# Performance work log

Hardware: AMD Instinct MI355X
Metric: run time of the kernel (lower is better)

The kernel has to match this reference:

```python
import jax, jax.numpy as jnp
import numpy as np
import math

DIM = 4096
N_HEADS = 32
HEAD_DIM = DIM // N_HEADS  # 128


def setup_inputs() -> dict:
    key = jax.random.key(0)
    ks = jax.random.split(key, 10)
    B, S, C = 2, 1024, 2048
    x = jax.random.normal(ks[0], (B, S, DIM), dtype=jnp.float32)
    freqs_cis = jax.random.normal(ks[1], (S, HEAD_DIM // 2), dtype=jnp.float32)
    mask = jnp.zeros((1, 1, S, C), dtype=jnp.float32)
    input_idexes = jnp.arange(S, dtype=jnp.int64) if jax.config.jax_enable_x64 else jnp.arange(S, dtype=jnp.int32)
    cache_k = jax.random.normal(ks[2], (B, C, N_HEADS, HEAD_DIM), dtype=jnp.float32) * 0.1
    cache_v = jax.random.normal(ks[3], (B, C, N_HEADS, HEAD_DIM), dtype=jnp.float32) * 0.1
    # Linear weights in torch layout [out_features, in_features], y = x @ W.T
    wq = jax.random.normal(ks[4], (DIM, DIM), dtype=jnp.float32) * 0.02
    wk = jax.random.normal(ks[5], (DIM, DIM), dtype=jnp.float32) * 0.02
    wv = jax.random.normal(ks[6], (DIM, DIM), dtype=jnp.float32) * 0.02
    wo = jax.random.normal(ks[7], (DIM, DIM), dtype=jnp.float32) * 0.02
    return {"x": x, "freqs_cis": freqs_cis, "mask": mask, "input_idexes": input_idexes,
            "cache_k": cache_k, "cache_v": cache_v, "wq": wq, "wk": wk, "wv": wv, "wo": wo}


def reference(x, freqs_cis, mask, input_idexes, cache_k, cache_v, wq, wk, wv, wo):
    B, S, D = x.shape
    H, hd = N_HEADS, HEAD_DIM
    # projections (torch Linear: x @ W.T)
    xq = jnp.einsum('bsd,ed->bse', x, wq).reshape(B, S, H, hd)
    # xk/xv are computed in the original forward but never used (cache-only attention)
    xk = jnp.einsum('bsd,ed->bse', x, wk).reshape(B, S, H, hd)  # noqa: F841
    xv = jnp.einsum('bsd,ed->bse', x, wv).reshape(B, S, H, hd)  # noqa: F841
    q = xq.transpose(0, 2, 1, 3)                 # [B,H,S,hd]
    keys = cache_k.transpose(0, 2, 1, 3)         # [B,H,C,hd]
    values = cache_v.transpose(0, 2, 1, 3)       # [B,H,C,hd]
    scores = jnp.einsum('bhse,bhce->bhsc', q, keys) / math.sqrt(hd)
    scores = scores + mask
    attn = jax.nn.softmax(scores.astype(jnp.float32), axis=-1).astype(q.dtype)
    out = jnp.einsum('bhsc,bhce->bhse', attn, values)  # [B,H,S,hd]
    out = out.transpose(0, 2, 1, 3).reshape(B, S, H * hd)
    return jnp.einsum('bse,de->bsd', out, wo)
```

## Files before the change

### kernel.cpp

```cpp
#include <hip/hip_runtime.h>
#include <hip/hip_bf16.h>
#include <stdint.h>


#define DIM   4096
#define NH    32
#define HD    128
#define BB    2
#define SS    1024
#define CC    2048

typedef __bf16 bf16x8 __attribute__((ext_vector_type(8)));
typedef float  f32x4  __attribute__((ext_vector_type(4)));

__device__ __forceinline__ unsigned short f2bf(float f) {
  union { __hip_bfloat16 h; unsigned short u; } cv;
  cv.h = __float2bfloat16(f);
  return cv.u;
}

__device__ __forceinline__ void gl_lds16(const void* g, void* l) {
  __builtin_amdgcn_global_load_lds(
      (__attribute__((address_space(1))) void*)(uintptr_t)(g),
      (__attribute__((address_space(3))) void*)(l), 16, 0, 0);
}

__global__ void conv_f32_bf16(const float* __restrict__ in, unsigned short* __restrict__ out, int n4) {
  int i = blockIdx.x * blockDim.x + threadIdx.x;
  int stride = gridDim.x * blockDim.x;
  for (; i < n4; i += stride) {
    float4 v = reinterpret_cast<const float4*>(in)[i];
    ushort4 o;
    o.x = f2bf(v.x); o.y = f2bf(v.y); o.z = f2bf(v.z); o.w = f2bf(v.w);
    reinterpret_cast<ushort4*>(out)[i] = o;
  }
}

__global__ void conv_k(const float* __restrict__ in, unsigned short* __restrict__ out) {
  const int total4 = BB * NH * CC * HD / 4;
  int i = blockIdx.x * blockDim.x + threadIdx.x;
  int stride = gridDim.x * blockDim.x;
  for (; i < total4; i += stride) {
    size_t o = (size_t)i * 4;
    int d   = (int)(o & (HD - 1));
    size_t r = o >> 7;
    int c   = (int)(r & (CC - 1));
    int bh  = (int)(r >> 11);
    int hh = bh & (NH - 1), bb = bh >> 5;
    float4 v = *reinterpret_cast<const float4*>(in + ((size_t)(bb * CC + c) * NH + hh) * HD + d);
    ushort4 u; u.x = f2bf(v.x); u.y = f2bf(v.y); u.z = f2bf(v.z); u.w = f2bf(v.w);
    *reinterpret_cast<ushort4*>(out + o) = u;
  }
}

__global__ void conv_v_t(const float* __restrict__ in, unsigned short* __restrict__ out) {
  __shared__ float tile[32][33];
  const int c0 = blockIdx.x * 32, d0 = blockIdx.y * 32;
  const int bh = blockIdx.z;
  const int hh = bh & (NH - 1), bb = bh >> 5;
  const int tx = threadIdx.x, ty = threadIdx.y;
#pragma unroll
  for (int i = 0; i < 4; ++i) {
    int c = c0 + ty + i * 8;
    tile[ty + i * 8][tx] = in[((size_t)(bb * CC + c) * NH + hh) * HD + d0 + tx];
  }
  __syncthreads();
#pragma unroll
  for (int i = 0; i < 4; ++i) {
    int d = d0 + ty + i * 8;
    out[((size_t)bh * HD + d) * CC + c0 + tx] = f2bf(tile[tx][ty + i * 8]);
  }
}

template <int OUT_BF16>
__global__ __launch_bounds__(256, 2) void gemm_bt(
    const unsigned short* __restrict__ A,
    const unsigned short* __restrict__ Bw,
    void* __restrict__ Cout,
    int M, int N, int K, float scale)
{
  __shared__ __align__(16) unsigned short As[128 * 32];
  __shared__ __align__(16) unsigned short Bs[128 * 32];
  const int t = threadIdx.x;
  const int w = t >> 6, lane = t & 63;
  const int wr = w >> 1, wc = w & 1;
  const int bm0 = blockIdx.y * 128, bn0 = blockIdx.x * 128;

  const unsigned short* aSrc = A  + (size_t)(bm0 + (t >> 2)) * K + (t & 3) * 8;
  const unsigned short* bSrc = Bw + (size_t)(bn0 + (t >> 2)) * K + (t & 3) * 8;
  char* aDst = (char*)As + w * 1024;
  char* bDst = (char*)Bs + w * 1024;
  const size_t half = (size_t)64 * K;

  f32x4 acc[4][4];
#pragma unroll
  for (int m = 0; m < 4; ++m)
#pragma unroll
    for (int n = 0; n < 4; ++n) acc[m][n] = (f32x4){0.f, 0.f, 0.f, 0.f};

  for (int k0 = 0; k0 < K; k0 += 32) {
    gl_lds16(aSrc,        aDst);
    gl_lds16(aSrc + half, aDst + 4096);
    gl_lds16(bSrc,        bDst);
    gl_lds16(bSrc + half, bDst + 4096);
    aSrc += 32; bSrc += 32;
    __syncthreads();

    bf16x8 af[4], bf[4];
#pragma unroll
    for (int m = 0; m < 4; ++m)
      af[m] = *(const bf16x8*)&As[(wr * 64 + m * 16 + (lane & 15)) * 32 + (lane >> 4) * 8];
#pragma unroll
    for (int n = 0; n < 4; ++n)
      bf[n] = *(const bf16x8*)&Bs[(wc * 64 + n * 16 + (lane & 15)) * 32 + (lane >> 4) * 8];
#pragma unroll
    for (int m = 0; m < 4; ++m)
#pragma unroll
      for (int n = 0; n < 4; ++n)
        acc[m][n] = __builtin_amdgcn_mfma_f32_16x16x32_bf16(af[m], bf[n], acc[m][n], 0, 0, 0);
    __syncthreads();
  }

  const int r0 = (lane >> 4) * 4, cl = lane & 15;
#pragma unroll
  for (int m = 0; m < 4; ++m) {
#pragma unroll
    for (int n = 0; n < 4; ++n) {
      int row = bm0 + wr * 64 + m * 16 + r0;
      int col = bn0 + wc * 64 + n * 16 + cl;
#pragma unroll
      for (int r = 0; r < 4; ++r) {
        float v = acc[m][n][r] * scale;
        if (OUT_BF16) ((unsigned short*)Cout)[(size_t)(row + r) * N + col] = f2bf(v);
        else          ((float*)Cout)[(size_t)(row + r) * N + col] = v;
      }
    }
  }
}

__global__ __launch_bounds__(256, 2) void attn_fwd(
    const unsigned short* __restrict__ Qb,
    const unsigned short* __restrict__ Kb,
    const unsigned short* __restrict__ Vtb,
    const float* __restrict__ mask,
    unsigned short* __restrict__ Ob)
{
  __shared__ __align__(16) unsigned short Ks[2][64 * 128];
  __shared__ __align__(16) unsigned short Vs[2][64 * 128];
  __shared__ __align__(16) unsigned short Ps[4][16 * 64];

  const int t = threadIdx.x, w = t >> 6, lane = t & 63;
  const int bid = blockIdx.x;
  const int qt = bid & 15, bh = bid >> 4;
  const int hh = bh & (NH - 1), bb = bh >> 5;
  const int q0 = qt * 64;
  const int l15 = lane & 15, g = lane >> 4;
  const int rb4 = g * 4;

  bf16x8 qf[4];
  {
    const unsigned short* qp = Qb + ((size_t)(bb * SS + q0 + w * 16 + l15)) * DIM + hh * HD + g * 8;
#pragma unroll
    for (int kk = 0; kk < 4; ++kk)
      qf[kk] = *(const bf16x8*)(qp + kk * 32);
  }

  const unsigned short* kSrc = Kb + ((size_t)bh * CC + (t >> 4)) * HD
                               + (((t & 15) ^ ((t >> 4) & 7)) * 8);
  const unsigned short* vSrc = Vtb + ((size_t)bh * HD + (t >> 3)) * CC
                               + (((t & 7) ^ ((t >> 3) & 7)) * 8);

  f32x4 acc_o[8];
#pragma unroll
  for (int i = 0; i < 8; ++i) acc_o[i] = (f32x4){0.f, 0.f, 0.f, 0.f};
  float m_run[4], l_run[4];
#pragma unroll
  for (int r = 0; r < 4; ++r) { m_run[r] = -1e30f; l_run[r] = 0.f; }

  const int swz = (lane & 7) << 3;
  const float LOG2E = 1.4426950408889634f;

  {
    char* kd = (char*)Ks[0] + w * 1024;
    char* vd = (char*)Vs[0] + w * 1024;
#pragma unroll
    for (int i = 0; i < 4; ++i) {
      gl_lds16(kSrc + (size_t)(i * 16) * HD, kd + i * 4096);
      gl_lds16(vSrc + (size_t)i * 32 * CC,   vd + i * 4096);
    }
  }
  __syncthreads();

  int cur = 0;
  for (int c0 = 0; c0 < CC; c0 += 64) {
    if (c0 + 64 < CC) {
      char* kd = (char*)Ks[cur ^ 1] + w * 1024;
      char* vd = (char*)Vs[cur ^ 1] + w * 1024;
#pragma unroll
      for (int i = 0; i < 4; ++i) {
        gl_lds16(kSrc + (size_t)(c0 + 64 + i * 16) * HD, kd + i * 4096);
        gl_lds16(vSrc + (size_t)i * 32 * CC + c0 + 64,   vd + i * 4096);
      }
    }

    float mk[4][4];
#pragma unroll
    for (int nf = 0; nf < 4; ++nf)
#pragma unroll
      for (int r = 0; r < 4; ++r)
        mk[nf][r] = mask[(size_t)(q0 + w * 16 + rb4 + r) * CC + c0 + nf * 16 + l15];

    f32x4 sc[4];
#pragma unroll
    for (int nf = 0; nf < 4; ++nf) sc[nf] = (f32x4){0.f, 0.f, 0.f, 0.f};
    __builtin_amdgcn_s_setprio(1);
#pragma unroll
    for (int kk = 0; kk < 4; ++kk) {
#pragma unroll
      for (int nf = 0; nf < 4; ++nf) {
        bf16x8 kf = *(const bf16x8*)&Ks[cur][((nf * 16 + l15) * 128 + kk * 32 + g * 8) ^ swz];
        sc[nf] = __builtin_amdgcn_mfma_f32_16x16x32_bf16(qf[kk], kf, sc[nf], 0, 0, 0);
      }
    }
    __builtin_amdgcn_s_setprio(0);

#pragma unroll
    for (int nf = 0; nf < 4; ++nf)
#pragma unroll
      for (int r = 0; r < 4; ++r)
        sc[nf][r] = fmaf(mk[nf][r], LOG2E, sc[nf][r]);

    int ok = 1;
    float pm[4];
#pragma unroll
    for (int r = 0; r < 4; ++r) {
      pm[r] = fmaxf(fmaxf(sc[0][r], sc[1][r]), fmaxf(sc[2][r], sc[3][r]));
      ok = ok && (pm[r] <= m_run[r] + 8.0f);
    }
    if (!__all(ok)) {
#pragma unroll
      for (int r = 0; r < 4; ++r) {
        float mx = pm[r];
#pragma unroll
        for (int d = 1; d < 16; d <<= 1)
          mx = fmaxf(mx, __shfl_xor(mx, d));
        float mn = fmaxf(m_run[r], mx);
        float corr = __builtin_amdgcn_exp2f(m_run[r] - mn);
        m_run[r] = mn;
        l_run[r] *= corr;
#pragma unroll
        for (int nd = 0; nd < 8; ++nd) acc_o[nd][r] *= corr;
      }
    }

#pragma unroll
    for (int r = 0; r < 4; ++r) {
      int rw = rb4 + r;
      int rsw = (rw & 7) << 3;
#pragma unroll
      for (int nf = 0; nf < 4; ++nf) {
        float p = __builtin_amdgcn_exp2f(sc[nf][r] - m_run[r]);
        l_run[r] += p;
        Ps[w][rw * 64 + ((nf * 16 + l15) ^ rsw)] = f2bf(p);
      }
    }

    __builtin_amdgcn_s_setprio(1);
#pragma unroll
    for (int kk = 0; kk < 2; ++kk) {
      bf16x8 pf = *(const bf16x8*)&Ps[w][(l15 * 64 + kk * 32 + g * 8) ^ swz];
#pragma unroll
      for (int nd = 0; nd < 8; ++nd) {
        bf16x8 vf = *(const bf16x8*)&Vs[cur][((nd * 16 + l15) * 64 + kk * 32 + g * 8) ^ swz];
        acc_o[nd] = __builtin_amdgcn_mfma_f32_16x16x32_bf16(pf, vf, acc_o[nd], 0, 0, 0);
      }
    }
    __builtin_amdgcn_s_setprio(0);
    __syncthreads();
    cur ^= 1;
  }

#pragma unroll
  for (int r = 0; r < 4; ++r)
#pragma unroll
    for (int d = 1; d < 16; d <<= 1)
      l_run[r] += __shfl_xor(l_run[r], d);

#pragma unroll
  for (int nd = 0; nd < 8; ++nd)
#pragma unroll
    for (int r = 0; r < 4; ++r) {
      float v = acc_o[nd][r] / l_run[r];
      int row = q0 + w * 16 + rb4 + r;
      Ob[(size_t)(bb * SS + row) * DIM + hh * HD + nd * 16 + l15] = f2bf(v);
    }
}

extern "C" void kernel_launch(void* const* d_in, const int* in_sizes, int n_in,
                              void* d_out, int out_size, void* d_ws, size_t ws_size,
                              hipStream_t stream) {
  const float* x       = (const float*)d_in[0];
  const float* mask    = (const float*)d_in[2];
  const float* cache_k = (const float*)d_in[4];
  const float* cache_v = (const float*)d_in[5];
  const float* wq      = (const float*)d_in[6];
  const float* wo      = (const float*)d_in[9];
  float* out = (float*)d_out;

  char* ws = (char*)d_ws;
  unsigned short* Wbf  = (unsigned short*)(ws);
  unsigned short* xbf  = (unsigned short*)(ws + 33554432);
  unsigned short* qbf  = (unsigned short*)(ws + 33554432 + 16777216);
  unsigned short* kbf  = (unsigned short*)(ws + 33554432 + 2 * 16777216);
  unsigned short* vtbf = (unsigned short*)(ws + 2 * 33554432 + 2 * 16777216);

  conv_f32_bf16<<<2048, 256, 0, stream>>>(x,  xbf, BB * SS * DIM / 4);
  conv_f32_bf16<<<2048, 256, 0, stream>>>(wq, Wbf, DIM * DIM / 4);
  dim3 gg(DIM / 128, (BB * SS) / 128);
  gemm_bt<1><<<gg, 256, 0, stream>>>(xbf, Wbf, qbf, BB * SS, DIM, DIM, 0.12751744682f);
  conv_k<<<2048, 256, 0, stream>>>(cache_k, kbf);
  conv_v_t<<<dim3(CC / 32, HD / 32, BB * NH), dim3(32, 8, 1), 0, stream>>>(cache_v, vtbf);
  attn_fwd<<<BB * NH * 16, 256, 0, stream>>>(qbf, kbf, vtbf, mask, xbf);
  conv_f32_bf16<<<2048, 256, 0, stream>>>(wo, Wbf, DIM * DIM / 4);
  gemm_bt<0><<<gg, 256, 0, stream>>>(xbf, Wbf, out, BB * SS, DIM, DIM, 1.0f);
}
```

Before: 407.5 us.

## Process 32 query rows per wave in attention to reuse K/V tiles

Each attention block now covers 128 query rows instead of 64, with every wave handling two 16-row fragments that share each K and V fragment loaded from LDS. This halves K/V global and LDS traffic per query row and halves the grid size. It also hoists the mask loads ahead of the async K/V prefetch, fenced by sched_barrier. The cost is roughly double the accumulator registers under launch_bounds(256,2), which risks spills or lower occupancy, and fewer blocks to spread across CUs.

Result: faster. 395.9 us (-2.9%).

```diff
diff --git a/kernel.cpp b/kernel.cpp
--- a/kernel.cpp
+++ b/kernel.cpp
@@ -147,22 +147,24 @@
 {
   __shared__ __align__(16) unsigned short Ks[2][64 * 128];
   __shared__ __align__(16) unsigned short Vs[2][64 * 128];
-  __shared__ __align__(16) unsigned short Ps[4][16 * 64];
+  __shared__ __align__(16) unsigned short Ps[4][32 * 64];
 
   const int t = threadIdx.x, w = t >> 6, lane = t & 63;
   const int bid = blockIdx.x;
-  const int qt = bid & 15, bh = bid >> 4;
+  const int qt = bid & 7, bh = bid >> 3;
   const int hh = bh & (NH - 1), bb = bh >> 5;
-  const int q0 = qt * 64;
+  const int q0 = qt * 128;
   const int l15 = lane & 15, g = lane >> 4;
   const int rb4 = g * 4;
 
-  bf16x8 qf[4];
-  {
-    const unsigned short* qp = Qb + ((size_t)(bb * SS + q0 + w * 16 + l15)) * DIM + hh * HD + g * 8;
+  bf16x8 qf[2][4];
+#pragma unroll
+  for (int rf = 0; rf < 2; ++rf) {
+    const unsigned short* qp = Qb + ((size_t)(bb * SS + q0 + w * 32 + rf * 16 + l15)) * DIM
+                               + hh * HD + g * 8;
 #pragma unroll
     for (int kk = 0; kk < 4; ++kk)
-      qf[kk] = *(const bf16x8*)(qp + kk * 32);
+      qf[rf][kk] = *(const bf16x8*)(qp + kk * 32);
   }
 
   const unsigned short* kSrc = Kb + ((size_t)bh * CC + (t >> 4)) * HD
@@ -170,12 +172,16 @@
   const unsigned short* vSrc = Vtb + ((size_t)bh * HD + (t >> 3)) * CC
                                + (((t & 7) ^ ((t >> 3) & 7)) * 8);
 
-  f32x4 acc_o[8];
-#pragma unroll
-  for (int i = 0; i < 8; ++i) acc_o[i] = (f32x4){0.f, 0.f, 0.f, 0.f};
-  float m_run[4], l_run[4];
-#pragma unroll
-  for (int r = 0; r < 4; ++r) { m_run[r] = -1e30f; l_run[r] = 0.f; }
+  f32x4 acc_o[2][8];
+#pragma unroll
+  for (int rf = 0; rf < 2; ++rf)
+#pragma unroll
+    for (int i = 0; i < 8; ++i) acc_o[rf][i] = (f32x4){0.f, 0.f, 0.f, 0.f};
+  float m_run[2][4], l_run[2][4];
+#pragma unroll
+  for (int rf = 0; rf < 2; ++rf)
+#pragma unroll
+    for (int r = 0; r < 4; ++r) { m_run[rf][r] = -1e30f; l_run[rf][r] = 0.f; }
 
   const int swz = (lane & 7) << 3;
   const float LOG2E = 1.4426950408889634f;
@@ -193,6 +199,17 @@
 
   int cur = 0;
   for (int c0 = 0; c0 < CC; c0 += 64) {
+    float mk[2][4][4];
+#pragma unroll
+    for (int rf = 0; rf < 2; ++rf)
+#pragma unroll
+      for (int nf = 0; nf < 4; ++nf)
+#pragma unroll
+        for (int r = 0; r < 4; ++r)
+          mk[rf][nf][r] = mask[(size_t)(q0 + w * 32 + rf * 16 + rb4 + r) * CC
+                               + c0 + nf * 16 + l15];
+    __builtin_amdgcn_sched_barrier(0);
+
     if (c0 + 64 < CC) {
       char* kd = (char*)Ks[cur ^ 1] + w * 1024;
       char* vd = (char*)Vs[cur ^ 1] + w * 1024;
@@ -202,77 +219,79 @@
         gl_lds16(vSrc + (size_t)i * 32 * CC + c0 + 64,   vd + i * 4096);
       }
     }
-
-    float mk[4][4];
-#pragma unroll
-    for (int nf = 0; nf < 4; ++nf)
-#pragma unroll
-      for (int r = 0; r < 4; ++r)
-        mk[nf][r] = mask[(size_t)(q0 + w * 16 + rb4 + r) * CC + c0 + nf * 16 + l15];
-
-    f32x4 sc[4];
-#pragma unroll
-    for (int nf = 0; nf < 4; ++nf) sc[nf] = (f32x4){0.f, 0.f, 0.f, 0.f};
+    __builtin_amdgcn_sched_barrier(0);
+
+    f32x4 sc[2][4];
+#pragma unroll
+    for (int rf = 0; rf < 2; ++rf)
+#pragma unroll
+      for (int nf = 0; nf < 4; ++nf) sc[rf][nf] = (f32x4){0.f, 0.f, 0.f, 0.f};
     __builtin_amdgcn_s_setprio(1);
 #pragma unroll
     for (int kk = 0; kk < 4; ++kk) {
 #pragma unroll
       for (int nf = 0; nf < 4; ++nf) {
         bf16x8 kf = *(const bf16x8*)&Ks[cur][((nf * 16 + l15) * 128 + kk * 32 + g * 8) ^ swz];
-        sc[nf] = __builtin_amdgcn_mfma_f32_16x16x32_bf16(qf[kk], kf, sc[nf], 0, 0, 0);
+        sc[0][nf] = __builtin_amdgcn_mfma_f32_16x16x32_bf16(qf[0][kk], kf, sc[0][nf], 0, 0, 0);
+        sc[1][nf] = __builtin_amdgcn_mfma_f32_16x16x32_bf16(qf[1][kk], kf, sc[1][nf], 0, 0, 0);
       }
     }
     __builtin_amdgcn_s_setprio(0);
 
 #pragma unroll
-    for (int nf = 0; nf < 4; ++nf)
-#pragma unroll
-      for (int r = 0; r < 4; ++r)
-        sc[nf][r] = fmaf(mk[nf][r], LOG2E, sc[nf][r]);
-
-    int ok = 1;
-    float pm[4];
-#pragma unroll
-    for (int r = 0; r < 4; ++r) {
-      pm[r] = fmaxf(fmaxf(sc[0][r], sc[1][r]), fmaxf(sc[2][r], sc[3][r]));
-      ok = ok && (pm[r] <= m_run[r] + 8.0f);
-    }
-    if (!__all(ok)) {
+    for (int rf = 0; rf < 2; ++rf) {
+#pragma unroll
+      for (int nf = 0; nf < 4; ++nf)
+#pragma unroll
+        for (int r = 0; r < 4; ++r)
+          sc[rf][nf][r] = fmaf(mk[rf][nf][r], LOG2E, sc[rf][nf][r]);
+
+      int ok = 1;
+      float pm[4];
 #pragma unroll
       for (int r = 0; r < 4; ++r) {
-        float mx = pm[r];
-#pragma unroll
-        for (int d = 1; d < 16; d <<= 1)
-          mx = fmaxf(mx, __shfl_xor(mx, d));
-        float mn = fmaxf(m_run[r], mx);
-        float corr = __builtin_amdgcn_exp2f(m_run[r] - mn);
-        m_run[r] = mn;
-        l_run[r] *= corr;
-#pragma unroll
-        for (int nd = 0; nd < 8; ++nd) acc_o[nd][r] *= corr;
-      }
-    }
-
-#pragma unroll
-    for (int r = 0; r < 4; ++r) {
-      int rw = rb4 + r;
-      int rsw = (rw & 7) << 3;
-#pragma unroll
-      for (int nf = 0; nf < 4; ++nf) {
-        float p = __builtin_amdgcn_exp2f(sc[nf][r] - m_run[r]);
-        l_run[r] += p;
-        Ps[w][rw * 64 + ((nf * 16 + l15) ^ rsw)] = f2bf(p);
+        pm[r] = fmaxf(fmaxf(sc[rf][0][r], sc[rf][1][r]), fmaxf(sc[rf][2][r], sc[rf][3][r]));
+        ok = ok && (pm[r] <= m_run[rf][r] + 8.0f);
+      }
+      if (!__all(ok)) {
+#pragma unroll
+        for (int r = 0; r < 4; ++r) {
+          float mx = pm[r];
+#pragma unroll
+          for (int d = 1; d < 16; d <<= 1)
+            mx = fmaxf(mx, __shfl_xor(mx, d));
+          float mn = fmaxf(m_run[rf][r], mx);
+          float corr = __builtin_amdgcn_exp2f(m_run[rf][r] - mn);
+          m_run[rf][r] = mn;
+          l_run[rf][r] *= corr;
+#pragma unroll
+          for (int nd = 0; nd < 8; ++nd) acc_o[rf][nd][r] *= corr;
+        }
+      }
+
+#pragma unroll
+      for (int r = 0; r < 4; ++r) {
+        int rw = rf * 16 + rb4 + r;
+        int rsw = (rw & 7) << 3;
+#pragma unroll
+        for (int nf = 0; nf < 4; ++nf) {
+          float p = __builtin_amdgcn_exp2f(sc[rf][nf][r] - m_run[rf][r]);
+          l_run[rf][r] += p;
+          Ps[w][rw * 64 + ((nf * 16 + l15) ^ rsw)] = f2bf(p);
+        }
       }
     }
 
     __builtin_amdgcn_s_setprio(1);
 #pragma unroll
     for (int kk = 0; kk < 2; ++kk) {
-      bf16x8 pf = *(const bf16x8*)&Ps[w][(l15 * 64 + kk * 32 + g * 8) ^ swz];
+      bf16x8 pf0 = *(const bf16x8*)&Ps[w][((0 * 16 + l15) * 64 + kk * 32 + g * 8) ^ swz];
+      bf16x8 pf1 = *(const bf16x8*)&Ps[w][((1 * 16 + l15) * 64 + kk * 32 + g * 8) ^ swz];
 #pragma unroll
       for (int nd = 0; nd < 8; ++nd) {
         bf16x8 vf = *(const bf16x8*)&Vs[cur][((nd * 16 + l15) * 64 + kk * 32 + g * 8) ^ swz];
-        acc_o[nd] = __builtin_amdgcn_mfma_f32_16x16x32_bf16(pf, vf, acc_o[nd], 0, 0, 0);
+        acc_o[0][nd] = __builtin_amdgcn_mfma_f32_16x16x32_bf16(pf0, vf, acc_o[0][nd], 0, 0, 0);
+        acc_o[1][nd] = __builtin_amdgcn_mfma_f32_16x16x32_bf16(pf1, vf, acc_o[1][nd], 0, 0, 0);
       }
     }
     __builtin_amdgcn_s_setprio(0);
@@ -281,19 +300,22 @@
   }
 
 #pragma unroll
-  for (int r = 0; r < 4; ++r)
-#pragma unroll
-    for (int d = 1; d < 16; d <<= 1)
-      l_run[r] += __shfl_xor(l_run[r], d);
-
-#pragma unroll
-  for (int nd = 0; nd < 8; ++nd)
-#pragma unroll
-    for (int r = 0; r < 4; ++r) {
-      float v = acc_o[nd][r] / l_run[r];
-      int row = q0 + w * 16 + rb4 + r;
-      Ob[(size_t)(bb * SS + row) * DIM + hh * HD + nd * 16 + l15] = f2bf(v);
-    }
+  for (int rf = 0; rf < 2; ++rf) {
+#pragma unroll
+    for (int r = 0; r < 4; ++r)
+#pragma unroll
+      for (int d = 1; d < 16; d <<= 1)
+        l_run[rf][r] += __shfl_xor(l_run[rf][r], d);
+
+#pragma unroll
+    for (int nd = 0; nd < 8; ++nd)
+#pragma unroll
+      for (int r = 0; r < 4; ++r) {
+        float v = acc_o[rf][nd][r] / l_run[rf][r];
+        int row = q0 + w * 32 + rf * 16 + rb4 + r;
+        Ob[(size_t)(bb * SS + row) * DIM + hh * HD + nd * 16 + l15] = f2bf(v);
+      }
+  }
 }
 
 extern "C" void kernel_launch(void* const* d_in, const int* in_sizes, int n_in,
@@ -320,7 +342,7 @@
   gemm_bt<1><<<gg, 256, 0, stream>>>(xbf, Wbf, qbf, BB * SS, DIM, DIM, 0.12751744682f);
   conv_k<<<2048, 256, 0, stream>>>(cache_k, kbf);
   conv_v_t<<<dim3(CC / 32, HD / 32, BB * NH), dim3(32, 8, 1), 0, stream>>>(cache_v, vtbf);
-  attn_fwd<<<BB * NH * 16, 256, 0, stream>>>(qbf, kbf, vtbf, mask, xbf);
+  attn_fwd<<<BB * NH * 8, 256, 0, stream>>>(qbf, kbf, vtbf, mask, xbf);
   conv_f32_bf16<<<2048, 256, 0, stream>>>(wo, Wbf, DIM * DIM / 4);
   gemm_bt<0><<<gg, 256, 0, stream>>>(xbf, Wbf, out, BB * SS, DIM, DIM, 1.0f);
 }
```

## Skip mask reads for all-zero tiles, widen attention blocks, swizzle GEMM tiles

Applied to the files above, without the earlier changes.

A new pre-pass kernel scans the mask in 128x64 tiles and writes a nonzero flag per tile into scratch space in the output buffer. The attention kernel reads these flags and loads and adds the mask only for tiles that have nonzero entries, removing the per-iteration mask global loads in the common case. Attention blocks grow to 512 threads covering 128 query rows so K/V tiles are shared by twice as many rows, and the GEMM remaps block indices so neighbouring workgroups share operand tiles in cache. The extra launch and the reuse of d_out as flag storage add overhead and depend on the output GEMM later overwriting those flags.

After: 450.1 us. 1.1x slower.

```diff
diff --git a/kernel.cpp b/kernel.cpp
--- a/kernel.cpp
+++ b/kernel.cpp
@@ -72,6 +72,25 @@
   }
 }
 
+__global__ void mask_flags(const float* __restrict__ mask, int* __restrict__ flags) {
+  __shared__ int s[4];
+  const int qt = blockIdx.x >> 5, ct = blockIdx.x & 31;
+  const int t = threadIdx.x, w = t >> 6;
+  const float4* m4 = (const float4*)mask;
+  int nz = 0;
+#pragma unroll
+  for (int i = 0; i < 8; ++i) {
+    int idx = i * 256 + t;
+    int row = idx >> 4, c4 = idx & 15;
+    float4 v = m4[(size_t)(qt * 128 + row) * (CC / 4) + ct * 16 + c4];
+    nz |= (v.x != 0.f) | (v.y != 0.f) | (v.z != 0.f) | (v.w != 0.f);
+  }
+  int wa = (int)__any(nz);
+  if ((t & 63) == 0) s[w] = wa;
+  __syncthreads();
+  if (t == 0) flags[qt * 32 + ct] = s[0] | s[1] | s[2] | s[3];
+}
+
 template <int OUT_BF16>
 __global__ __launch_bounds__(256, 2) void gemm_bt(
     const unsigned short* __restrict__ A,
@@ -84,7 +103,10 @@
   const int t = threadIdx.x;
   const int w = t >> 6, lane = t & 63;
   const int wr = w >> 1, wc = w & 1;
-  const int bm0 = blockIdx.y * 128, bn0 = blockIdx.x * 128;
+  const int nwg  = gridDim.x * gridDim.y;
+  const int flat = blockIdx.y * gridDim.x + blockIdx.x;
+  const int swzb = (flat & 7) * (nwg >> 3) + (flat >> 3);
+  const int bm0 = (swzb / gridDim.x) * 128, bn0 = (swzb % gridDim.x) * 128;
 
   const unsigned short* aSrc = A  + (size_t)(bm0 + (t >> 2)) * K + (t & 3) * 8;
   const unsigned short* bSrc = Bw + (size_t)(bn0 + (t >> 2)) * K + (t & 3) * 8;
@@ -138,28 +160,30 @@
   }
 }
 
-__global__ __launch_bounds__(256, 2) void attn_fwd(
+__global__ __launch_bounds__(512, 4) void attn_fwd(
     const unsigned short* __restrict__ Qb,
     const unsigned short* __restrict__ Kb,
     const unsigned short* __restrict__ Vtb,
     const float* __restrict__ mask,
+    const int* __restrict__ Mf,
     unsigned short* __restrict__ Ob)
 {
   __shared__ __align__(16) unsigned short Ks[2][64 * 128];
   __shared__ __align__(16) unsigned short Vs[2][64 * 128];
-  __shared__ __align__(16) unsigned short Ps[4][16 * 64];
+  __shared__ __align__(16) unsigned short Ps[8][16 * 64];
 
   const int t = threadIdx.x, w = t >> 6, lane = t & 63;
-  const int bid = blockIdx.x;
-  const int qt = bid & 15, bh = bid >> 4;
+  const int lg = (blockIdx.x & 7) * 64 + (blockIdx.x >> 3);
+  const int qt = lg & 7, bh = lg >> 3;
   const int hh = bh & (NH - 1), bb = bh >> 5;
-  const int q0 = qt * 64;
+  const int q0 = qt * 128;
   const int l15 = lane & 15, g = lane >> 4;
   const int rb4 = g * 4;
 
   bf16x8 qf[4];
   {
-    const unsigned short* qp = Qb + ((size_t)(bb * SS + q0 + w * 16 + l15)) * DIM + hh * HD + g * 8;
+    const unsigned short* qp = Qb + ((size_t)(bb * SS + q0 + w * 16 + l15)) * DIM
+                               + hh * HD + g * 8;
 #pragma unroll
     for (int kk = 0; kk < 4; ++kk)
       qf[kk] = *(const bf16x8*)(qp + kk * 32);
@@ -180,35 +204,33 @@
   const int swz = (lane & 7) << 3;
   const float LOG2E = 1.4426950408889634f;
 
+  int mflag = Mf[qt * 32];
   {
     char* kd = (char*)Ks[0] + w * 1024;
     char* vd = (char*)Vs[0] + w * 1024;
 #pragma unroll
-    for (int i = 0; i < 4; ++i) {
-      gl_lds16(kSrc + (size_t)(i * 16) * HD, kd + i * 4096);
-      gl_lds16(vSrc + (size_t)i * 32 * CC,   vd + i * 4096);
+    for (int i = 0; i < 2; ++i) {
+      gl_lds16(kSrc + (size_t)(i * 32) * HD, kd + i * 8192);
+      gl_lds16(vSrc + (size_t)i * 64 * CC,   vd + i * 8192);
     }
   }
   __syncthreads();
 
   int cur = 0;
   for (int c0 = 0; c0 < CC; c0 += 64) {
+    const int ct = c0 >> 6;
+    int nextFlag = (ct < 31) ? Mf[qt * 32 + ct + 1] : 0;
+
     if (c0 + 64 < CC) {
       char* kd = (char*)Ks[cur ^ 1] + w * 1024;
       char* vd = (char*)Vs[cur ^ 1] + w * 1024;
 #pragma unroll
-      for (int i = 0; i < 4; ++i) {
-        gl_lds16(kSrc + (size_t)(c0 + 64 + i * 16) * HD, kd + i * 4096);
-        gl_lds16(vSrc + (size_t)i * 32 * CC + c0 + 64,   vd + i * 4096);
-      }
-    }
-
-    float mk[4][4];
-#pragma unroll
-    for (int nf = 0; nf < 4; ++nf)
-#pragma unroll
-      for (int r = 0; r < 4; ++r)
-        mk[nf][r] = mask[(size_t)(q0 + w * 16 + rb4 + r) * CC + c0 + nf * 16 + l15];
+      for (int i = 0; i < 2; ++i) {
+        gl_lds16(kSrc + (size_t)(c0 + 64 + i * 32) * HD, kd + i * 8192);
+        gl_lds16(vSrc + (size_t)i * 64 * CC + c0 + 64,   vd + i * 8192);
+      }
+    }
+    __builtin_amdgcn_sched_barrier(0);
 
     f32x4 sc[4];
 #pragma unroll
@@ -224,11 +246,14 @@
     }
     __builtin_amdgcn_s_setprio(0);
 
-#pragma unroll
-    for (int nf = 0; nf < 4; ++nf)
-#pragma unroll
-      for (int r = 0; r < 4; ++r)
-        sc[nf][r] = fmaf(mk[nf][r], LOG2E, sc[nf][r]);
+    if (mflag) {
+#pragma unroll
+      for (int nf = 0; nf < 4; ++nf)
+#pragma unroll
+        for (int r = 0; r < 4; ++r)
+          sc[nf][r] = fmaf(mask[(size_t)(q0 + w * 16 + rb4 + r) * CC + c0 + nf * 16 + l15],
+                           LOG2E, sc[nf][r]);
+    }
 
     int ok = 1;
     float pm[4];
@@ -278,6 +303,7 @@
     __builtin_amdgcn_s_setprio(0);
     __syncthreads();
     cur ^= 1;
+    mflag = nextFlag;
   }
 
 #pragma unroll
@@ -313,6 +339,7 @@
   unsigned short* qbf  = (unsigned short*)(ws + 33554432 + 16777216);
   unsigned short* kbf  = (unsigned short*)(ws + 33554432 + 2 * 16777216);
   unsigned short* vtbf = (unsigned short*)(ws + 2 * 33554432 + 2 * 16777216);
+  int* mflags = (int*)d_out;
 
   conv_f32_bf16<<<2048, 256, 0, stream>>>(x,  xbf, BB * SS * DIM / 4);
   conv_f32_bf16<<<2048, 256, 0, stream>>>(wq, Wbf, DIM * DIM / 4);
@@ -320,7 +347,8 @@
   gemm_bt<1><<<gg, 256, 0, stream>>>(xbf, Wbf, qbf, BB * SS, DIM, DIM, 0.12751744682f);
   conv_k<<<2048, 256, 0, stream>>>(cache_k, kbf);
   conv_v_t<<<dim3(CC / 32, HD / 32, BB * NH), dim3(32, 8, 1), 0, stream>>>(cache_v, vtbf);
-  attn_fwd<<<BB * NH * 16, 256, 0, stream>>>(qbf, kbf, vtbf, mask, xbf);
+  mask_flags<<<256, 256, 0, stream>>>(mask, mflags);
+  attn_fwd<<<BB * NH * 8, 512, 0, stream>>>(qbf, kbf, vtbf, mask, mflags, xbf);
   conv_f32_bf16<<<2048, 256, 0, stream>>>(wo, Wbf, DIM * DIM / 4);
   gemm_bt<0><<<gg, 256, 0, stream>>>(xbf, Wbf, out, BB * SS, DIM, DIM, 1.0f);
 }
```
